# Performance work log

Measured on AMD Instinct MI355X. Metric: run time of the kernel, lower is better.

## Reference

```python
import jax, jax.numpy as jnp
import numpy as np
import math

V, T, D, N, H, DFF = 32000, 1024, 1024, 6, 16, 4096
DK = D // H
EPS = 1e-6


def setup_inputs() -> dict:
    key = jax.random.key(0)
    ks = jax.random.split(key, 20)
    s = 0.02
    B = 2
    return {
        "idx": jax.random.randint(ks[0], (B, T), 0, V, dtype=jnp.int32),
        "emb": jax.random.normal(ks[1], (V, D), jnp.float32) * s,
        # attention projections, stored [in, out] so y = x @ W
        "Wq": jax.random.normal(ks[2], (N, D, D), jnp.float32) * s,
        "Wk": jax.random.normal(ks[3], (N, D, D), jnp.float32) * s,
        "Wv": jax.random.normal(ks[4], (N, D, D), jnp.float32) * s,
        "Wo": jax.random.normal(ks[5], (N, D, D), jnp.float32) * s,
        "ln1_a": jnp.ones((N, D), jnp.float32),
        "ln1_b": jnp.zeros((N, D), jnp.float32),
        "ln2_a": jnp.ones((N, D), jnp.float32),
        "ln2_b": jnp.zeros((N, D), jnp.float32),
        "W1": jax.random.normal(ks[6], (N, D, DFF), jnp.float32) * s,
        "b1": jnp.zeros((N, DFF), jnp.float32),
        "W2": jax.random.normal(ks[7], (N, DFF, D), jnp.float32) * s,
        "b2": jnp.zeros((N, D), jnp.float32),
        "fnorm_a": jnp.ones((D,), jnp.float32),
        "fnorm_b": jnp.zeros((D,), jnp.float32),
        "Wp": jax.random.normal(ks[8], (D, V), jnp.float32) * s,
        "bp": jnp.zeros((V,), jnp.float32),
    }


def _layernorm(x, a, b):
    # torch .std() uses Bessel correction (ddof=1); denom is (std + eps), not sqrt(var+eps)
    mean = x.mean(axis=-1, keepdims=True)
    std = jnp.std(x, axis=-1, keepdims=True, ddof=1)
    return a * (x - mean) / (std + EPS) + b


def _pos_encoding(t, d):
    pos = jnp.arange(t, dtype=jnp.float32)[:, None]
    div = jnp.exp(jnp.arange(0, d, 2, dtype=jnp.float32) * (-math.log(10000.0) / d))
    pe = jnp.zeros((t, d), jnp.float32)
    pe = pe.at[:, 0::2].set(jnp.sin(pos * div))
    pe = pe.at[:, 1::2].set(jnp.cos(pos * div))
    return pe


def _forward(idx, emb, Wq, Wk, Wv, Wo, ln1_a, ln1_b, ln2_a, ln2_b,
             W1, b1, W2, b2, fnorm_a, fnorm_b, Wp, bp):
    B, Tc = idx.shape
    x = emb[idx] * math.sqrt(D) + _pos_encoding(Tc, D)  # [B,T,D]
    causal = jnp.tril(jnp.ones((Tc, Tc), bool))  # [T,T]

    def block(x, p):
        wq, wk, wv, wo, a1, c1, a2, c2, w1, bb1, w2, bb2 = p
        h_in = _layernorm(x, a1, c1)
        q = (h_in @ wq).reshape(B, Tc, H, DK).transpose(0, 2, 1, 3)
        k = (h_in @ wk).reshape(B, Tc, H, DK).transpose(0, 2, 1, 3)
        v = (h_in @ wv).reshape(B, Tc, H, DK).transpose(0, 2, 1, 3)
        scores = jnp.einsum('bhqd,bhkd->bhqk', q, k) / math.sqrt(DK)
        scores = jnp.where(causal, scores, -1e9)
        attn = jax.nn.softmax(scores, axis=-1)
        o = jnp.einsum('bhqk,bhkd->bhqd', attn, v)
        o = o.transpose(0, 2, 1, 3).reshape(B, Tc, D) @ wo
        x = x + o
        h2 = _layernorm(x, a2, c2)
        ff = jax.nn.relu(h2 @ w1 + bb1) @ w2 + bb2
        x = x + ff
        return x, None

    x, _ = jax.lax.scan(block, x, (Wq, Wk, Wv, Wo, ln1_a, ln1_b, ln2_a, ln2_b, W1, b1, W2, b2))
    x = _layernorm(x, fnorm_a, fnorm_b)
    logits = x @ Wp + bp  # [B,T,V]
    return logits


def reference(idx, emb, Wq, Wk, Wv, Wo, ln1_a, ln1_b, ln2_a, ln2_b,
              W1, b1, W2, b2, fnorm_a, fnorm_b, Wp, bp):
    return _forward(idx, emb, Wq, Wk, Wv, Wo, ln1_a, ln1_b, ln2_a, ln2_b,
                    W1, b1, W2, b2, fnorm_a, fnorm_b, Wp, bp)
```

## Files before the change

### kernel.cpp

```cpp
#include <hip/hip_runtime.h>
#include <hip/hip_bf16.h>
#include <math.h>

#define VOCAB 32000
#define TSEQ 1024
#define DMODEL 1024
#define NLAYERS 6
#define NHEADS 16
#define DFF 4096
#define DKH 64
#define BATCH 2
#define MROWS (BATCH * TSEQ)
#define LN_EPS 1e-6f
#define QKVS 3072

typedef unsigned short u16;
typedef __attribute__((ext_vector_type(8))) short short8v;
typedef __attribute__((ext_vector_type(4))) float f32x4;

__device__ __forceinline__ u16 f2bb(float f) {
    __hip_bfloat16 h = __float2bfloat16(f);
    u16 u; __builtin_memcpy(&u, &h, 2); return u;
}

__device__ __forceinline__ void gload16(const void* g, void* l) {
    __builtin_amdgcn_global_load_lds(
        (const __attribute__((address_space(1))) unsigned int*)g,
        (__attribute__((address_space(3))) unsigned int*)l, 16, 0, 0);
}

__global__ void embed_kernel(const int* __restrict__ idx,
                             const float* __restrict__ emb,
                             float* __restrict__ x) {
    int i = blockIdx.x * blockDim.x + threadIdx.x;
    if (i >= MROWS * DMODEL) return;
    int row = i / DMODEL;
    int d = i - row * DMODEL;
    int t = row % TSEQ;
    int tok = idx[row];
    float e = emb[(size_t)tok * DMODEL + d] * 32.0f;
    float freq = expf(-(float)(d & ~1) * (9.210340371976184f / (float)DMODEL));
    float ang = (float)t * freq;
    float pe = (d & 1) ? cosf(ang) : sinf(ang);
    x[i] = e + pe;
}

template<bool OB16>
__global__ void __launch_bounds__(256) ln_kernel(const float* __restrict__ x,
                                                 const float* __restrict__ a,
                                                 const float* __restrict__ b,
                                                 void* __restrict__ yv) {
    __shared__ float red[8];
    int row = blockIdx.x;
    int tid = threadIdx.x;
    float4 v = ((const float4*)(x + (size_t)row * DMODEL))[tid];
    float s = v.x + v.y + v.z + v.w;
    #pragma unroll
    for (int off = 32; off; off >>= 1) s += __shfl_xor(s, off, 64);
    if ((tid & 63) == 0) red[tid >> 6] = s;
    __syncthreads();
    float mean = (red[0] + red[1] + red[2] + red[3]) * (1.0f / DMODEL);
    float dx = v.x - mean, dy = v.y - mean, dz = v.z - mean, dw = v.w - mean;
    float ss = dx * dx + dy * dy + dz * dz + dw * dw;
    #pragma unroll
    for (int off = 32; off; off >>= 1) ss += __shfl_xor(ss, off, 64);
    if ((tid & 63) == 0) red[4 + (tid >> 6)] = ss;
    __syncthreads();
    float var = (red[4] + red[5] + red[6] + red[7]) * (1.0f / (DMODEL - 1));
    float inv = 1.0f / (sqrtf(var) + LN_EPS);
    const float4 a4 = ((const float4*)a)[tid];
    const float4 b4 = ((const float4*)b)[tid];
    float o0 = a4.x * dx * inv + b4.x;
    float o1 = a4.y * dy * inv + b4.y;
    float o2 = a4.z * dz * inv + b4.z;
    float o3 = a4.w * dw * inv + b4.w;
    if (OB16) {
        ushort4 o; o.x = f2bb(o0); o.y = f2bb(o1); o.z = f2bb(o2); o.w = f2bb(o3);
        ((ushort4*)((u16*)yv + (size_t)row * DMODEL))[tid] = o;
    } else {
        float4 o; o.x = o0; o.y = o1; o.z = o2; o.w = o3;
        ((float4*)((float*)yv + (size_t)row * DMODEL))[tid] = o;
    }
}

__global__ void __launch_bounds__(256) convT(const float* __restrict__ in,
                                             u16* __restrict__ out, int K, int N) {
    __shared__ float t[32][33];
    in  += (size_t)blockIdx.z * K * N;
    out += (size_t)blockIdx.z * K * N;
    const int tx = threadIdx.x, ty = threadIdx.y;
    const int n0 = blockIdx.x * 32, k0 = blockIdx.y * 32;
    #pragma unroll
    for (int i = 0; i < 4; ++i)
        t[ty + i * 8][tx] = in[(size_t)(k0 + ty + i * 8) * N + n0 + tx];
    __syncthreads();
    #pragma unroll
    for (int i = 0; i < 4; ++i)
        out[(size_t)(n0 + ty + i * 8) * K + k0 + tx] = f2bb(t[tx][ty + i * 8]);
}

__global__ void __launch_bounds__(256) convQKVO(const float* __restrict__ Wq,
                                                const float* __restrict__ Wk,
                                                const float* __restrict__ Wv,
                                                const float* __restrict__ Wo,
                                                u16* __restrict__ WqkvT,
                                                u16* __restrict__ WoT) {
    __shared__ float t[32][33];
    const int z = blockIdx.z, L = z >> 2, p = z & 3;
    const size_t MM = (size_t)DMODEL * DMODEL;
    const float* in = (p == 0 ? Wq : p == 1 ? Wk : p == 2 ? Wv : Wo) + (size_t)L * MM;
    u16* out = (p < 3) ? (WqkvT + (size_t)L * 3 * MM + (size_t)p * MM)
                       : (WoT + (size_t)L * MM);
    const int tx = threadIdx.x, ty = threadIdx.y;
    const int n0 = blockIdx.x * 32, k0 = blockIdx.y * 32;
    #pragma unroll
    for (int i = 0; i < 4; ++i)
        t[ty + i * 8][tx] = in[(size_t)(k0 + ty + i * 8) * DMODEL + n0 + tx];
    __syncthreads();
    #pragma unroll
    for (int i = 0; i < 4; ++i)
        out[(size_t)(n0 + ty + i * 8) * DMODEL + k0 + tx] = f2bb(t[tx][ty + i * 8]);
}

template<int BMT, bool BIAS, bool RELU, bool RES, bool OB16>
__global__ void __launch_bounds__(256) gemm_mfma(
    const u16* __restrict__ A, const u16* __restrict__ Bt,
    const float* __restrict__ bias, const float* res,
    void* outp, int N, int K)
{
    constexpr int MR = BMT / 32;
    constexpr int AR = BMT / 64;
    __shared__ u16 Alds[2][BMT * 32];
    __shared__ u16 Blds[2][128 * 32];
    const int tid = threadIdx.x;
    const int w = tid >> 6, lane = tid & 63;
    const int wr = w >> 1, wc = w & 1;
    const size_t bm = (size_t)blockIdx.y * BMT;
    const size_t bn = (size_t)blockIdx.x * 128;
    const int srow = (w << 4) + (lane >> 2);
    const int scol = (((lane & 3) ^ ((lane >> 3) & 3)) << 3);
    const int fr = lane & 15, fq = lane >> 4;
    const int aswz = ((fq ^ ((fr >> 1) & 3)) << 3);

    f32x4 acc[MR][4];
    #pragma unroll
    for (int m = 0; m < MR; ++m)
        #pragma unroll
        for (int n = 0; n < 4; ++n)
            acc[m][n] = (f32x4){0.f, 0.f, 0.f, 0.f};

    #pragma unroll
    for (int li = 0; li < AR; ++li)
        gload16(A + (bm + li * 64 + srow) * K + scol, Alds[0] + li * 2048 + w * 512);
    #pragma unroll
    for (int li = 0; li < 2; ++li)
        gload16(Bt + (bn + li * 64 + srow) * K + scol, Blds[0] + li * 2048 + w * 512);
    __syncthreads();

    int cur = 0;
    for (int k0 = 0; k0 < K; k0 += 32) {
        if (k0 + 32 < K) {
            const int nb = cur ^ 1;
            #pragma unroll
            for (int li = 0; li < AR; ++li)
                gload16(A + (bm + li * 64 + srow) * K + k0 + 32 + scol, Alds[nb] + li * 2048 + w * 512);
            #pragma unroll
            for (int li = 0; li < 2; ++li)
                gload16(Bt + (bn + li * 64 + srow) * K + k0 + 32 + scol, Blds[nb] + li * 2048 + w * 512);
        }
        short8v a[MR], b[4];
        #pragma unroll
        for (int m = 0; m < MR; ++m)
            a[m] = *(const short8v*)(Alds[cur] + (wr * (BMT / 2) + m * 16 + fr) * 32 + aswz);
        #pragma unroll
        for (int n = 0; n < 4; ++n)
            b[n] = *(const short8v*)(Blds[cur] + (wc * 64 + n * 16 + fr) * 32 + aswz);
        #pragma unroll
        for (int m = 0; m < MR; ++m)
            #pragma unroll
            for (int n = 0; n < 4; ++n)
                acc[m][n] = __builtin_amdgcn_mfma_f32_16x16x32_bf16(a[m], b[n], acc[m][n], 0, 0, 0);
        __syncthreads();
        cur ^= 1;
    }

    #pragma unroll
    for (int n = 0; n < 4; ++n) {
        const size_t col = bn + wc * 64 + n * 16 + fr;
        const float bv = BIAS ? bias[col] : 0.f;
        #pragma unroll
        for (int m = 0; m < MR; ++m) {
            #pragma unroll
            for (int r = 0; r < 4; ++r) {
                const size_t row = bm + wr * (BMT / 2) + m * 16 + fq * 4 + r;
                float v = acc[m][n][r] + bv;
                if (RELU) v = fmaxf(v, 0.f);
                if (RES)  v += res[row * N + col];
                if (OB16) ((u16*)outp)[row * N + col] = f2bb(v);
                else      ((float*)outp)[row * N + col] = v;
            }
        }
    }
}

__global__ void __launch_bounds__(256) attn_flash(const u16* __restrict__ qkv,
                                                  u16* __restrict__ o) {
    __shared__ u16 Klds[64 * 64];
    __shared__ u16 Vt[64 * 64];
    __shared__ u16 Plds[4][16 * 72];

    const int tid = threadIdx.x;
    const int w = tid >> 6, lane = tid & 63;
    const int fr = lane & 15, fq = lane >> 4;
    const int qt = gridDim.x - 1 - blockIdx.x;
    const int h = blockIdx.y, b = blockIdx.z;
    const int qbase = qt * 64 + w * 16;
    const size_t rowbase = (size_t)b * TSEQ;
    const int hd = h * DKH;

    const int rk = tid >> 3;
    const int c8 = (tid & 7) << 3;

    const u16* qrow = qkv + (rowbase + qbase + fr) * QKVS + hd;
    const short8v qf0 = *(const short8v*)(qrow + fq * 8);
    const short8v qf1 = *(const short8v*)(qrow + 32 + fq * 8);

    float m[4], l[4];
    f32x4 oa[4];
    #pragma unroll
    for (int r = 0; r < 4; ++r) { m[r] = -1e30f; l[r] = 0.f; }
    #pragma unroll
    for (int nd = 0; nd < 4; ++nd) oa[nd] = (f32x4){0.f, 0.f, 0.f, 0.f};

    short8v ka0, ka1, va0, va1;
    short8v kb0, kb1, vb0, vb1;

    auto load_set = [&](int j0, short8v& k0v, short8v& k1v, short8v& v0v, short8v& v1v) {
        const size_t gk = (rowbase + j0 + rk) * QKVS + hd + c8 + 1024;
        k0v = *(const short8v*)(qkv + gk);
        k1v = *(const short8v*)(qkv + gk + (size_t)32 * QKVS);
        const size_t gv = (rowbase + j0 + 2 * rk) * QKVS + hd + c8 + 2048;
        v0v = *(const short8v*)(qkv + gv);
        v1v = *(const short8v*)(qkv + gv + QKVS);
    };
    auto stage_set = [&](const short8v& k0v, const short8v& k1v,
                         const short8v& v0v, const short8v& v1v) {
        const int kb0b = (rk * 128 + c8 * 2) ^ ((rk & 7) << 4);
        *(short8v*)((char*)Klds + kb0b) = k0v;
        const int r2 = rk + 32;
        const int kb1b = (r2 * 128 + c8 * 2) ^ ((r2 & 7) << 4);
        *(short8v*)((char*)Klds + kb1b) = k1v;
        #pragma unroll
        for (int i = 0; i < 8; ++i) {
            const int vrow = c8 + i;
            const int slot = (((2 * rk) >> 3) + (vrow >> 3)) & 7;
            unsigned int pair = ((unsigned int)(u16)v0v[i]) |
                                (((unsigned int)(u16)v1v[i]) << 16);
            *(unsigned int*)(&Vt[vrow * 64 + slot * 8 + ((2 * rk) & 7)]) = pair;
        }
    };
    auto do_tile = [&](int t) {
        const int j0 = t * 64;
        f32x4 s[4];
        __builtin_amdgcn_s_setprio(1);
        #pragma unroll
        for (int ct = 0; ct < 4; ++ct) {
            const int krow = ct * 16 + fr;
            const int swz = (krow & 7) << 4;
            short8v k0 = *(const short8v*)((char*)Klds + ((krow * 128 + fq * 16) ^ swz));
            short8v k1 = *(const short8v*)((char*)Klds + ((krow * 128 + 64 + fq * 16) ^ swz));
            f32x4 a = (f32x4){0.f, 0.f, 0.f, 0.f};
            a = __builtin_amdgcn_mfma_f32_16x16x32_bf16(qf0, k0, a, 0, 0, 0);
            a = __builtin_amdgcn_mfma_f32_16x16x32_bf16(qf1, k1, a, 0, 0, 0);
            s[ct] = a;
        }
        __builtin_amdgcn_s_setprio(0);

        float c[4];
        #pragma unroll
        for (int r = 0; r < 4; ++r) {
            const int qg = qbase + fq * 4 + r;
            float sv[4];
            #pragma unroll
            for (int ct = 0; ct < 4; ++ct) {
                sv[ct] = s[ct][r] * 0.125f;
                if (j0 + ct * 16 + fr > qg) sv[ct] = -1e30f;
            }
            float mx = fmaxf(fmaxf(sv[0], sv[1]), fmaxf(sv[2], sv[3]));
            mx = fmaxf(mx, __shfl_xor(mx, 1, 64));
            mx = fmaxf(mx, __shfl_xor(mx, 2, 64));
            mx = fmaxf(mx, __shfl_xor(mx, 4, 64));
            mx = fmaxf(mx, __shfl_xor(mx, 8, 64));
            const float mn = fmaxf(m[r], mx);
            c[r] = __expf(m[r] - mn);
            m[r] = mn;
            float p0 = __expf(sv[0] - mn);
            float p1 = __expf(sv[1] - mn);
            float p2 = __expf(sv[2] - mn);
            float p3 = __expf(sv[3] - mn);
            float rs = (p0 + p1) + (p2 + p3);
            rs += __shfl_xor(rs, 1, 64);
            rs += __shfl_xor(rs, 2, 64);
            rs += __shfl_xor(rs, 4, 64);
            rs += __shfl_xor(rs, 8, 64);
            l[r] = l[r] * c[r] + rs;
            u16* prow = &Plds[w][(fq * 4 + r) * 72];
            prow[fr]      = f2bb(p0);
            prow[16 + fr] = f2bb(p1);
            prow[32 + fr] = f2bb(p2);
            prow[48 + fr] = f2bb(p3);
        }
        #pragma unroll
        for (int nd = 0; nd < 4; ++nd)
            #pragma unroll
            for (int r = 0; r < 4; ++r)
                oa[nd][r] *= c[r];
        asm volatile("s_waitcnt lgkmcnt(0)" ::: "memory");
        __builtin_amdgcn_sched_barrier(0);

        __builtin_amdgcn_s_setprio(1);
        #pragma unroll
        for (int ks = 0; ks < 2; ++ks) {
            const short8v pf = *(const short8v*)(&Plds[w][fr * 72 + ks * 32 + fq * 8]);
            #pragma unroll
            for (int nd = 0; nd < 4; ++nd) {
                const int vrow = nd * 16 + fr;
                const int slot = (ks * 4 + fq + (vrow >> 3)) & 7;
                const short8v vf = *(const short8v*)(&Vt[vrow * 64 + slot * 8]);
                oa[nd] = __builtin_amdgcn_mfma_f32_16x16x32_bf16(pf, vf, oa[nd], 0, 0, 0);
            }
        }
        __builtin_amdgcn_s_setprio(0);
    };

    load_set(0, ka0, ka1, va0, va1);
    int t = 0;
    for (;;) {
        stage_set(ka0, ka1, va0, va1);
        __syncthreads();
        if (t < qt) load_set((t + 1) * 64, kb0, kb1, vb0, vb1);
        do_tile(t);
        __syncthreads();
        if (++t > qt) break;
        stage_set(kb0, kb1, vb0, vb1);
        __syncthreads();
        if (t < qt) load_set((t + 1) * 64, ka0, ka1, va0, va1);
        do_tile(t);
        __syncthreads();
        if (++t > qt) break;
    }

    #pragma unroll
    for (int r = 0; r < 4; ++r) {
        const float inv = 1.0f / l[r];
        u16* orow = o + (rowbase + qbase + fq * 4 + r) * DMODEL + hd;
        #pragma unroll
        for (int nd = 0; nd < 4; ++nd)
            orow[nd * 16 + fr] = f2bb(oa[nd][r] * inv);
    }
}

#define FBM 64
#define FBN 64
#define FBK 16
__global__ void __launch_bounds__(256) gemm_f32(
    const float* __restrict__ A, const float* __restrict__ Bw,
    const float* __restrict__ bias, float* outp, int N, int K)
{
    __shared__ float As[FBK][FBM];
    __shared__ float Bs[FBK][FBN];
    const int bm = blockIdx.y * FBM, bn = blockIdx.x * FBN;
    const int tid = threadIdx.x;
    const int tr = (tid >> 4) << 2, tc = (tid & 15) << 2;
    const int am = tid >> 2, ak = (tid & 3) << 2;
    const int bk = tid >> 4, bn4 = (tid & 15) << 2;
    float acc[4][4] = {};
    const float* Ap = A + (size_t)(bm + am) * K + ak;
    const float* Bp = Bw + (size_t)bk * N + bn + bn4;
    for (int k0 = 0; k0 < K; k0 += FBK) {
        float4 av = *(const float4*)(Ap + k0);
        float4 bv = *(const float4*)(Bp + (size_t)k0 * N);
        As[ak + 0][am] = av.x; As[ak + 1][am] = av.y; As[ak + 2][am] = av.z; As[ak + 3][am] = av.w;
        *(float4*)&Bs[bk][bn4] = bv;
        __syncthreads();
        #pragma unroll
        for (int kk = 0; kk < FBK; ++kk) {
            float4 a4 = *(const float4*)&As[kk][tr];
            float4 b4 = *(const float4*)&Bs[kk][tc];
            acc[0][0] += a4.x*b4.x; acc[0][1] += a4.x*b4.y; acc[0][2] += a4.x*b4.z; acc[0][3] += a4.x*b4.w;
            acc[1][0] += a4.y*b4.x; acc[1][1] += a4.y*b4.y; acc[1][2] += a4.y*b4.z; acc[1][3] += a4.y*b4.w;
            acc[2][0] += a4.z*b4.x; acc[2][1] += a4.z*b4.y; acc[2][2] += a4.z*b4.z; acc[2][3] += a4.z*b4.w;
            acc[3][0] += a4.w*b4.x; acc[3][1] += a4.w*b4.y; acc[3][2] += a4.w*b4.z; acc[3][3] += a4.w*b4.w;
        }
        __syncthreads();
    }
    #pragma unroll
    for (int i = 0; i < 4; ++i) {
        int row = bm + tr + i;
        float4 o;
        o.x = acc[i][0] + bias[bn + tc + 0];
        o.y = acc[i][1] + bias[bn + tc + 1];
        o.z = acc[i][2] + bias[bn + tc + 2];
        o.w = acc[i][3] + bias[bn + tc + 3];
        *(float4*)(outp + (size_t)row * N + bn + tc) = o;
    }
}

extern "C" void kernel_launch(void* const* d_in, const int* in_sizes, int n_in,
                              void* d_out, int out_size, void* d_ws, size_t ws_size,
                              hipStream_t stream) {
    const int* idx = (const int*)d_in[0];
    const float* emb = (const float*)d_in[1];
    const float* Wq = (const float*)d_in[2];
    const float* Wk = (const float*)d_in[3];
    const float* Wv = (const float*)d_in[4];
    const float* Wo = (const float*)d_in[5];
    const float* ln1a = (const float*)d_in[6];
    const float* ln1b = (const float*)d_in[7];
    const float* ln2a = (const float*)d_in[8];
    const float* ln2b = (const float*)d_in[9];
    const float* W1 = (const float*)d_in[10];
    const float* b1 = (const float*)d_in[11];
    const float* W2 = (const float*)d_in[12];
    const float* b2 = (const float*)d_in[13];
    const float* fa = (const float*)d_in[14];
    const float* fb = (const float*)d_in[15];
    const float* Wp = (const float*)d_in[16];
    const float* bp = (const float*)d_in[17];
    float* out = (float*)d_out;

    const size_t MD = (size_t)MROWS * DMODEL;
    const size_t MM = (size_t)DMODEL * DMODEL;
    u16* U = (u16*)out;
    u16* qkv = U;
    u16* ob = U + 3 * MD;
    u16* hb = U + 4 * MD;
    float* x = (float*)(U + 5 * MD);
    u16* ff = U + 7 * MD;
    u16* WqkvT = U + 12 * MD;
    u16* WoT = U + 21 * MD;
    u16* W1T = U + 24 * MD;
    u16* W2T = U + 36 * MD;

    const bool pathA = ws_size >= (size_t)68 * 1024 * 1024 + 256;
    u16* WpT = (u16*)d_ws;
    u16* h2b = (u16*)((char*)d_ws + (size_t)64 * 1024 * 1024);
    float* hF = (float*)d_ws;

    dim3 cblk(32, 8);
    convQKVO<<<dim3(32, 32, 24), cblk, 0, stream>>>(Wq, Wk, Wv, Wo, WqkvT, WoT);
    convT<<<dim3(128, 32, 6), cblk, 0, stream>>>(W1, W1T, DMODEL, DFF);
    convT<<<dim3(32, 128, 6), cblk, 0, stream>>>(W2, W2T, DFF, DMODEL);
    if (pathA) convT<<<dim3(1000, 32, 1), cblk, 0, stream>>>(Wp, WpT, DMODEL, VOCAB);

    embed_kernel<<<(MROWS * DMODEL + 255) / 256, 256, 0, stream>>>(idx, emb, x);

    for (int L = 0; L < NLAYERS; ++L) {
        ln_kernel<true><<<MROWS, 256, 0, stream>>>(x, ln1a + (size_t)L * DMODEL, ln1b + (size_t)L * DMODEL, hb);
        gemm_mfma<128, false, false, false, true><<<dim3(24, 16), 256, 0, stream>>>(
            hb, WqkvT + (size_t)L * 3 * MM, nullptr, nullptr, qkv, QKVS, DMODEL);
        attn_flash<<<dim3(TSEQ / 64, NHEADS, BATCH), 256, 0, stream>>>(qkv, ob);
        gemm_mfma<64, false, false, true, false><<<dim3(8, 32), 256, 0, stream>>>(
            ob, WoT + (size_t)L * MM, nullptr, x, x, DMODEL, DMODEL);
        ln_kernel<true><<<MROWS, 256, 0, stream>>>(x, ln2a + (size_t)L * DMODEL, ln2b + (size_t)L * DMODEL, hb);
        gemm_mfma<128, true, true, false, true><<<dim3(32, 16), 256, 0, stream>>>(
            hb, W1T + (size_t)L * DFF * DMODEL, b1 + (size_t)L * DFF, nullptr, ff, DFF, DMODEL);
        gemm_mfma<64, true, false, true, false><<<dim3(8, 32), 256, 0, stream>>>(
            ff, W2T + (size_t)L * DFF * DMODEL, b2 + (size_t)L * DMODEL, x, x, DMODEL, DFF);
    }

    if (pathA) {
        ln_kernel<true><<<MROWS, 256, 0, stream>>>(x, fa, fb, h2b);
        gemm_mfma<128, true, false, false, false><<<dim3(250, 16), 256, 0, stream>>>(
            h2b, WpT, bp, nullptr, out, VOCAB, DMODEL);
    } else {
        ln_kernel<false><<<MROWS, 256, 0, stream>>>(x, fa, fb, hF);
        gemm_f32<<<dim3(VOCAB / FBN, MROWS / FBM), 256, 0, stream>>>(hF, Wp, bp, out, VOCAB, DMODEL);
    }
}
```

Baseline: 1.676 ms.

## Triple-buffer GEMM LDS tiles with explicit vmcnt waits for deeper prefetch

Changes the MFMA GEMM main loop from double to triple buffering in LDS. Tile t+2 is prefetched while tile t is computed, and s_waitcnt vmcnt with a count is used in place of a full __syncthreads drain, so two tiles of loads stay in flight. This aims to hide global-load latency better. In exchange it uses 50% more LDS per block, which may lower occupancy, and the manual waitcnt/barrier reasoning is fragile: the clamped duplicate prefetch of the last tile rewrites buffers near the end of the loop.

```diff
diff --git a/kernel.cpp b/kernel.cpp
--- a/kernel.cpp
+++ b/kernel.cpp
@@ -17,6 +17,8 @@
 typedef unsigned short u16;
 typedef __attribute__((ext_vector_type(8))) short short8v;
 typedef __attribute__((ext_vector_type(4))) float f32x4;
+
+#define WAITCNT_VM(N) asm volatile("s_waitcnt vmcnt(" #N ")" ::: "memory")
 
 __device__ __forceinline__ u16 f2bb(float f) {
     __hip_bfloat16 h = __float2bfloat16(f);
@@ -130,8 +132,8 @@
 {
     constexpr int MR = BMT / 32;
     constexpr int AR = BMT / 64;
-    __shared__ u16 Alds[2][BMT * 32];
-    __shared__ u16 Blds[2][128 * 32];
+    __shared__ u16 Alds[3][BMT * 32];
+    __shared__ u16 Blds[3][128 * 32];
     const int tid = threadIdx.x;
     const int w = tid >> 6, lane = tid & 63;
     const int wr = w >> 1, wc = w & 1;
@@ -149,40 +151,46 @@
         for (int n = 0; n < 4; ++n)
             acc[m][n] = (f32x4){0.f, 0.f, 0.f, 0.f};
 
-    #pragma unroll
-    for (int li = 0; li < AR; ++li)
-        gload16(A + (bm + li * 64 + srow) * K + scol, Alds[0] + li * 2048 + w * 512);
-    #pragma unroll
-    for (int li = 0; li < 2; ++li)
-        gload16(Bt + (bn + li * 64 + srow) * K + scol, Blds[0] + li * 2048 + w * 512);
-    __syncthreads();
-
-    int cur = 0;
-    for (int k0 = 0; k0 < K; k0 += 32) {
-        if (k0 + 32 < K) {
-            const int nb = cur ^ 1;
-            #pragma unroll
-            for (int li = 0; li < AR; ++li)
-                gload16(A + (bm + li * 64 + srow) * K + k0 + 32 + scol, Alds[nb] + li * 2048 + w * 512);
-            #pragma unroll
-            for (int li = 0; li < 2; ++li)
-                gload16(Bt + (bn + li * 64 + srow) * K + k0 + 32 + scol, Blds[nb] + li * 2048 + w * 512);
-        }
+    auto issue = [&](int kt, int buf) {
+        const int k0 = kt * 32;
+        #pragma unroll
+        for (int li = 0; li < AR; ++li)
+            gload16(A + (bm + li * 64 + srow) * K + k0 + scol, Alds[buf] + li * 2048 + w * 512);
+        #pragma unroll
+        for (int li = 0; li < 2; ++li)
+            gload16(Bt + (bn + li * 64 + srow) * K + k0 + scol, Blds[buf] + li * 2048 + w * 512);
+    };
+
+    const int nt = K / 32;
+    issue(0, 0);
+    issue(1, 1);
+    if constexpr (AR == 2) WAITCNT_VM(4); else WAITCNT_VM(3);
+    __builtin_amdgcn_s_barrier();
+    __builtin_amdgcn_sched_barrier(0);
+
+    for (int t = 0; t < nt; ++t) {
+        const int pf = (t + 2 < nt) ? t + 2 : nt - 1;
+        issue(pf, (t + 2) % 3);
+        if constexpr (AR == 2) WAITCNT_VM(8); else WAITCNT_VM(6);
+        __builtin_amdgcn_s_barrier();
+        __builtin_amdgcn_sched_barrier(0);
+        const u16* Ab = Alds[t % 3];
+        const u16* Bb = Blds[t % 3];
         short8v a[MR], b[4];
         #pragma unroll
         for (int m = 0; m < MR; ++m)
-            a[m] = *(const short8v*)(Alds[cur] + (wr * (BMT / 2) + m * 16 + fr) * 32 + aswz);
+            a[m] = *(const short8v*)(Ab + (wr * (BMT / 2) + m * 16 + fr) * 32 + aswz);
         #pragma unroll
         for (int n = 0; n < 4; ++n)
-            b[n] = *(const short8v*)(Blds[cur] + (wc * 64 + n * 16 + fr) * 32 + aswz);
+            b[n] = *(const short8v*)(Bb + (wc * 64 + n * 16 + fr) * 32 + aswz);
         #pragma unroll
         for (int m = 0; m < MR; ++m)
             #pragma unroll
             for (int n = 0; n < 4; ++n)
                 acc[m][n] = __builtin_amdgcn_mfma_f32_16x16x32_bf16(a[m], b[n], acc[m][n], 0, 0, 0);
-        __syncthreads();
-        cur ^= 1;
-    }
+        __builtin_amdgcn_s_barrier();
+    }
+    WAITCNT_VM(0);
 
     #pragma unroll
     for (int n = 0; n < 4; ++n) {
```

Result: no change. 1.669 ms (-0.4%).
